# Kernel tuning notes

Measured on AMD Instinct MI355X. Metric: run time of the kernel, lower is better.

## Reference

```python
import jax, jax.numpy as jnp
import numpy as np

NUM_RANGES = 700
K = 250
IN_DIM = 7      # 1 power + 3 elevation embed + 3 azimuth embed
HID = 32        # Q/K hidden dim
NUM_LAYERS = 2
SCALE = 1.0 / (HID ** 0.5)


def setup_inputs() -> dict:
    key = jax.random.key(0)
    ks = jax.random.split(key, 12)
    N = NUM_RANGES * K
    inp = {
        "power_vals": jax.random.normal(ks[0], (N, 1), dtype=jnp.float32),
        "ele_indices": jax.random.randint(ks[1], (N,), 0, 37),
        "azi_indices": jax.random.randint(ks[2], (N,), 0, 107),
        # learned parameters
        "ele_emb": jax.random.normal(ks[3], (37, 3), dtype=jnp.float32),
        "azi_emb": jax.random.normal(ks[4], (107, 3), dtype=jnp.float32),
        # per-layer Q/K/V linear params, stacked over layers
        "Wq": jax.random.normal(ks[5], (NUM_LAYERS, IN_DIM, HID), dtype=jnp.float32) * 0.2,
        "bq": jax.random.normal(ks[6], (NUM_LAYERS, HID), dtype=jnp.float32) * 0.02,
        "Wk": jax.random.normal(ks[7], (NUM_LAYERS, IN_DIM, HID), dtype=jnp.float32) * 0.2,
        "bk": jax.random.normal(ks[8], (NUM_LAYERS, HID), dtype=jnp.float32) * 0.02,
        "Wv": jax.random.normal(ks[9], (NUM_LAYERS, IN_DIM, 1), dtype=jnp.float32) * 0.2,
        "bv": jax.random.normal(ks[10], (NUM_LAYERS, 1), dtype=jnp.float32) * 0.02,
    }
    return inp


def reference(power_vals, ele_indices, azi_indices, ele_emb, azi_emb, Wq, bq, Wk, bk, Wv, bv):
    # x: [R, K, 1]
    x = power_vals.reshape(NUM_RANGES, K, -1)
    # embedding lookups: [R, K, 3]
    e = ele_emb[ele_indices.reshape(NUM_RANGES, K)].astype(jnp.float32)
    a = azi_emb[azi_indices.reshape(NUM_RANGES, K)].astype(jnp.float32)
    for i in range(NUM_LAYERS):
        h = jnp.concatenate([x, e, a], axis=-1)           # [R, K, 7]
        q = h @ Wq[i] + bq[i]                             # [R, K, 32]
        k = h @ Wk[i] + bk[i]                             # [R, K, 32]
        v = h @ Wv[i] + bv[i]                             # [R, K, 1]
        scores = jnp.einsum("rqd,rkd->rqk", q, k) * SCALE  # [R, K, K]
        probs = jax.nn.softmax(scores, axis=-1)
        x = jnp.einsum("rqk,rkd->rqd", probs, v)          # [R, K, 1]
    return x.reshape(NUM_RANGES * K, 1)
```

## Files before the change

### kernel.cpp

```cpp
#include <hip/hip_runtime.h>
#include <hip/hip_fp16.h>

#define NR 700
#define KK 250
#define HID 32

typedef unsigned int uint32;
typedef _Float16 f16x8 __attribute__((ext_vector_type(8)));
typedef float f32x4 __attribute__((ext_vector_type(4)));
typedef _Float16 hpair __attribute__((ext_vector_type(2)));

#if __has_builtin(__builtin_amdgcn_exp2f)
#define EXP2F(x) __builtin_amdgcn_exp2f(x)
#else
#define EXP2F(x) exp2f(x)
#endif

__device__ __forceinline__ uint32 packh2(float lo, float hi) {
    hpair p; p.x = (_Float16)lo; p.y = (_Float16)hi;
    return __builtin_bit_cast(uint32, p);
}
__device__ __forceinline__ f16x8 u4f16(uint4 u) { return __builtin_bit_cast(f16x8, u); }

__device__ __forceinline__ void compute_weights(
    int wt, int l,
    const float* __restrict__ Wq, const float* __restrict__ bq,
    const float* __restrict__ Wk,
    const float* __restrict__ Wv, const float* __restrict__ bv,
    float (*Msh)[7], float* wsh, float* wvsh, float SC2Q)
{
    const float* wq = Wq + l * 7 * HID;
    const float* wk = Wk + l * 7 * HID;
    if (wt < 49) {
        int c = wt / 7, cp = wt % 7;
        float s = 0.f;
        #pragma unroll 8
        for (int d = 0; d < HID; ++d) s = fmaf(wq[c * HID + d], wk[cp * HID + d], s);
        Msh[c][cp] = s * SC2Q;
    } else if (wt < 56) {
        int cp = wt - 49;
        float s = 0.f;
        #pragma unroll 8
        for (int d = 0; d < HID; ++d) s = fmaf(bq[l * HID + d], wk[cp * HID + d], s);
        wsh[cp] = s * SC2Q;
    } else if (wt < 63) {
        wvsh[wt - 56] = Wv[l * 7 + (wt - 56)];
    } else if (wt == 63) {
        wvsh[7] = bv[l];
    }
}

__global__ __launch_bounds__(256, 4) void mlra_kernel(
    const float* __restrict__ power,
    const int*   __restrict__ ele_idx,
    const int*   __restrict__ azi_idx,
    const float* __restrict__ ele_emb,
    const float* __restrict__ azi_emb,
    const float* __restrict__ Wq,
    const float* __restrict__ bq,
    const float* __restrict__ Wk,
    const float* __restrict__ bk,
    const float* __restrict__ Wv,
    const float* __restrict__ bv,
    float* __restrict__ out)
{
    __shared__ uint4 hh[256];
    __shared__ uint4 tt[256];
    __shared__ uint4 vpk[8][4];
    __shared__ float Msh[2][7][7];
    __shared__ float wsh[2][7];
    __shared__ float wvsh[2][8];

    const int r    = blockIdx.x;
    const int tid  = threadIdx.x;
    const int lane = tid & 63;
    const int wid  = tid >> 6;
    const int col  = lane & 15;
    const int grp  = lane >> 4;

    const float SC2Q = 0.17677669529663687f * 1.4426950408889634f * 0.25f;

    {
        float hv[7];
        if (tid < KK) {
            int g = r * KK + tid;
            hv[0] = power[g];
            int ei = ele_idx[g];
            int ai = azi_idx[g];
            hv[1] = ele_emb[ei * 3 + 0];
            hv[2] = ele_emb[ei * 3 + 1];
            hv[3] = ele_emb[ei * 3 + 2];
            hv[4] = azi_emb[ai * 3 + 0];
            hv[5] = azi_emb[ai * 3 + 1];
            hv[6] = azi_emb[ai * 3 + 2];
        } else {
            #pragma unroll
            for (int c = 0; c < 7; ++c) hv[c] = 0.f;
        }
        uint4 u;
        u.x = packh2(hv[0], hv[1]);
        u.y = packh2(hv[2], hv[3]);
        u.z = packh2(hv[4], hv[5]);
        u.w = packh2(hv[6], 0.f);
        hh[tid] = u;
    }
    if (tid < 128) {
        compute_weights(tid & 63, tid >> 6, Wq, bq, Wk, Wv, bv,
                        Msh[tid >> 6], wsh[tid >> 6], wvsh[tid >> 6], SC2Q);
    }
    __syncthreads();

    const f32x4 cz = {0.f, 0.f, 0.f, 0.f};
    float x0 = 0.f, x1 = 0.f, x2 = 0.f, x3 = 0.f;

    for (int l = 0; l < 2; ++l) {
        {
            uint4 u = hh[tid];
            hpair pa = __builtin_bit_cast(hpair, u.x);
            hpair pb = __builtin_bit_cast(hpair, u.y);
            hpair pc = __builtin_bit_cast(hpair, u.z);
            hpair pd = __builtin_bit_cast(hpair, u.w);
            float hv[7] = {(float)pa.x, (float)pa.y, (float)pb.x, (float)pb.y,
                           (float)pc.x, (float)pc.y, (float)pd.x};
            float tv[7];
            #pragma unroll
            for (int cp = 0; cp < 7; ++cp) {
                float s = wsh[l][cp];
                #pragma unroll
                for (int c = 0; c < 7; ++c) s = fmaf(hv[c], Msh[l][c][cp], s);
                tv[cp] = s;
            }
            float v = wvsh[l][7];
            #pragma unroll
            for (int c = 0; c < 7; ++c) v = fmaf(hv[c], wvsh[l][c], v);
            uint4 t4;
            t4.x = packh2(tv[0], tv[1]);
            t4.y = packh2(tv[2], tv[3]);
            t4.z = packh2(tv[4], tv[5]);
            t4.w = packh2(tv[6], 0.f);
            tt[tid] = t4;
            int jtp = tid >> 5, halfsel = (tid >> 4) & 1, grow = (tid >> 2) & 3, rg = tid & 3;
            reinterpret_cast<_Float16*>(vpk)[(jtp * 4 + grow) * 8 + halfsel * 4 + rg] =
                (_Float16)((tid < KK) ? v : 0.f);
        }
        __syncthreads();

        f16x8 bt0 = u4f16(tt[(wid * 4 + 0) * 16 + col]);
        f16x8 bt1 = u4f16(tt[(wid * 4 + 1) * 16 + col]);
        f16x8 bt2 = u4f16(tt[(wid * 4 + 2) * 16 + col]);
        f16x8 bt3 = u4f16(tt[(wid * 4 + 3) * 16 + col]);

        float ss0 = 0.f, oo0 = 0.f, ss1 = 0.f, oo1 = 0.f;
        float ss2 = 0.f, oo2 = 0.f, ss3 = 0.f, oo3 = 0.f;
        #pragma unroll 1
        for (int jtp = 0; jtp < 8; ++jtp) {
            f16x8 ahe = u4f16(hh[jtp * 32 + col]);
            f16x8 aho = u4f16(hh[jtp * 32 + 16 + col]);
            uint4 vq  = vpk[jtp][grp];
            hpair v01e = __builtin_bit_cast(hpair, vq.x);
            hpair v23e = __builtin_bit_cast(hpair, vq.y);
            hpair v01o = __builtin_bit_cast(hpair, vq.z);
            hpair v23o = __builtin_bit_cast(hpair, vq.w);
            float ve0 = (float)v01e.x, ve1 = (float)v01e.y;
            float ve2 = (float)v23e.x, ve3 = (float)v23e.y;
            float vo0 = (float)v01o.x, vo1 = (float)v01o.y;
            float vo2 = (float)v23o.x, vo3 = (float)v23o.y;

            f32x4 ce0 = __builtin_amdgcn_mfma_f32_16x16x32_f16(ahe, bt0, cz, 0, 0, 0);
            f32x4 ce1 = __builtin_amdgcn_mfma_f32_16x16x32_f16(ahe, bt1, cz, 0, 0, 0);
            f32x4 ce2 = __builtin_amdgcn_mfma_f32_16x16x32_f16(ahe, bt2, cz, 0, 0, 0);
            f32x4 ce3 = __builtin_amdgcn_mfma_f32_16x16x32_f16(ahe, bt3, cz, 0, 0, 0);
            f32x4 co0 = __builtin_amdgcn_mfma_f32_16x16x32_f16(aho, bt0, cz, 0, 0, 0);
            f32x4 co1 = __builtin_amdgcn_mfma_f32_16x16x32_f16(aho, bt1, cz, 0, 0, 0);
            f32x4 co2 = __builtin_amdgcn_mfma_f32_16x16x32_f16(aho, bt2, cz, 0, 0, 0);
            f32x4 co3 = __builtin_amdgcn_mfma_f32_16x16x32_f16(aho, bt3, cz, 0, 0, 0);

            #define ACC(ct, vv0, vv1, vv2, vv3, SS, OO)                         \
            {                                                                    \
                float p0 = EXP2F(ct[0]); float p1 = EXP2F(ct[1]);                \
                float p2 = EXP2F(ct[2]); float p3 = EXP2F(ct[3]);                \
                SS += (p0 + p1) + (p2 + p3);                                     \
                OO = fmaf(p0, vv0, OO); OO = fmaf(p1, vv1, OO);                  \
                OO = fmaf(p2, vv2, OO); OO = fmaf(p3, vv3, OO);                  \
            }
            ACC(ce0, ve0, ve1, ve2, ve3, ss0, oo0)
            ACC(ce1, ve0, ve1, ve2, ve3, ss1, oo1)
            ACC(ce2, ve0, ve1, ve2, ve3, ss2, oo2)
            ACC(ce3, ve0, ve1, ve2, ve3, ss3, oo3)
            ACC(co0, vo0, vo1, vo2, vo3, ss0, oo0)
            ACC(co1, vo0, vo1, vo2, vo3, ss1, oo1)
            ACC(co2, vo0, vo1, vo2, vo3, ss2, oo2)
            ACC(co3, vo0, vo1, vo2, vo3, ss3, oo3)
            #undef ACC
        }
        {
            int ex = 4 * grp - 6;
            ex = ex < 0 ? 0 : (ex > 4 ? 4 : ex);
            float exf = (float)ex;
            ss0 -= exf; ss1 -= exf; ss2 -= exf; ss3 -= exf;
        }

        ss0 += __shfl_xor(ss0, 16); ss0 += __shfl_xor(ss0, 32);
        oo0 += __shfl_xor(oo0, 16); oo0 += __shfl_xor(oo0, 32);
        ss1 += __shfl_xor(ss1, 16); ss1 += __shfl_xor(ss1, 32);
        oo1 += __shfl_xor(oo1, 16); oo1 += __shfl_xor(oo1, 32);
        ss2 += __shfl_xor(ss2, 16); ss2 += __shfl_xor(ss2, 32);
        oo2 += __shfl_xor(oo2, 16); oo2 += __shfl_xor(oo2, 32);
        ss3 += __shfl_xor(ss3, 16); ss3 += __shfl_xor(ss3, 32);
        oo3 += __shfl_xor(oo3, 16); oo3 += __shfl_xor(oo3, 32);
        x0 = oo0 / ss0; x1 = oo1 / ss1; x2 = oo2 / ss2; x3 = oo3 / ss3;

        if (l == 0) {
            __syncthreads();
            if (grp == 0) {
                int i0 = (wid * 4 + 0) * 16 + col;
                int i1 = (wid * 4 + 1) * 16 + col;
                int i2 = (wid * 4 + 2) * 16 + col;
                int i3 = (wid * 4 + 3) * 16 + col;
                _Float16* hhf = reinterpret_cast<_Float16*>(hh);
                hhf[i0 * 8] = (_Float16)x0;
                hhf[i1 * 8] = (_Float16)x1;
                hhf[i2 * 8] = (_Float16)x2;
                if (i3 < KK) hhf[i3 * 8] = (_Float16)x3;
            }
            __syncthreads();
        }
    }

    if (grp == 0) {
        int i0 = (wid * 4 + 0) * 16 + col;
        int i1 = (wid * 4 + 1) * 16 + col;
        int i2 = (wid * 4 + 2) * 16 + col;
        int i3 = (wid * 4 + 3) * 16 + col;
        out[r * KK + i0] = x0;
        out[r * KK + i1] = x1;
        out[r * KK + i2] = x2;
        if (i3 < KK) out[r * KK + i3] = x3;
    }
}

extern "C" void kernel_launch(void* const* d_in, const int* in_sizes, int n_in,
                              void* d_out, int out_size, void* d_ws, size_t ws_size,
                              hipStream_t stream) {
    const float* power   = (const float*)d_in[0];
    const int*   ele     = (const int*)d_in[1];
    const int*   azi     = (const int*)d_in[2];
    const float* ele_emb = (const float*)d_in[3];
    const float* azi_emb = (const float*)d_in[4];
    const float* Wq      = (const float*)d_in[5];
    const float* bq      = (const float*)d_in[6];
    const float* Wk      = (const float*)d_in[7];
    const float* bk      = (const float*)d_in[8];
    const float* Wv      = (const float*)d_in[9];
    const float* bv      = (const float*)d_in[10];
    float* outp = (float*)d_out;
    (void)bk;

    hipLaunchKernelGGL(mlra_kernel, dim3(NR), dim3(256), 0, stream,
                       power, ele, azi, ele_emb, azi_emb, Wq, bq, Wk, bk, Wv, bv, outp);
}
```

Measured before the change: 23.37 us.

## Compute softmax P·V and row sums with an extra MFMA instead of scalar FMAs

Exponentiated scores are packed to fp16 and multiplied by a B operand holding V in column 0 and ones in column 1, so one MFMA yields both the weighted sum and the softmax denominator. This replaces per-lane scalar FMA accumulation and cross-lane xor-shuffle reductions with matrix-core work and a single shuffle per output. It adds fp16 rounding of probabilities (round-toward-zero) and leaves a dead macro in the code.

```diff
diff --git a/kernel.cpp b/kernel.cpp
--- a/kernel.cpp
+++ b/kernel.cpp
@@ -21,6 +21,9 @@
     return __builtin_bit_cast(uint32, p);
 }
 __device__ __forceinline__ f16x8 u4f16(uint4 u) { return __builtin_bit_cast(f16x8, u); }
+__device__ __forceinline__ uint32 pkrtz(float a, float b) {
+    return __builtin_bit_cast(uint32, __builtin_amdgcn_cvt_pkrtz(a, b));
+}
 
 __device__ __forceinline__ void compute_weights(
     int wt, int l,
@@ -66,7 +69,7 @@
 {
     __shared__ uint4 hh[256];
     __shared__ uint4 tt[256];
-    __shared__ uint4 vpk[8][4];
+    __shared__ _Float16 vB[8][32];
     __shared__ float Msh[2][7][7];
     __shared__ float wsh[2][7];
     __shared__ float wvsh[2][8];
@@ -76,7 +79,7 @@
     const int lane = tid & 63;
     const int wid  = tid >> 6;
     const int col  = lane & 15;
-    const int grp  = lane >> 4;
+    const int kg   = lane >> 4;
 
     const float SC2Q = 0.17677669529663687f * 1.4426950408889634f * 0.25f;
 
@@ -111,7 +114,7 @@
     __syncthreads();
 
     const f32x4 cz = {0.f, 0.f, 0.f, 0.f};
-    float x0 = 0.f, x1 = 0.f, x2 = 0.f, x3 = 0.f;
+    float xs[4];
 
     for (int l = 0; l < 2; ++l) {
         {
@@ -139,9 +142,10 @@
             t4.z = packh2(tv[4], tv[5]);
             t4.w = packh2(tv[6], 0.f);
             tt[tid] = t4;
-            int jtp = tid >> 5, halfsel = (tid >> 4) & 1, grow = (tid >> 2) & 3, rg = tid & 3;
-            reinterpret_cast<_Float16*>(vpk)[(jtp * 4 + grow) * 8 + halfsel * 4 + rg] =
-                (_Float16)((tid < KK) ? v : 0.f);
+            int jtp = tid >> 5, j32 = tid & 31;
+            int kgw = (j32 & 15) >> 2;
+            int e   = (j32 & 3) + ((j32 >> 4) << 2);
+            vB[jtp][kgw * 8 + e] = (_Float16)((tid < KK) ? v : 0.f);
         }
         __syncthreads();
 
@@ -150,21 +154,20 @@
         f16x8 bt2 = u4f16(tt[(wid * 4 + 2) * 16 + col]);
         f16x8 bt3 = u4f16(tt[(wid * 4 + 3) * 16 + col]);
 
-        float ss0 = 0.f, oo0 = 0.f, ss1 = 0.f, oo1 = 0.f;
-        float ss2 = 0.f, oo2 = 0.f, ss3 = 0.f, oo3 = 0.f;
+        f32x4 cv0 = cz, cv1 = cz, cv2 = cz, cv3 = cz;
+        const uint32 onesm = 0x3C003C00u;
+
         #pragma unroll 1
         for (int jtp = 0; jtp < 8; ++jtp) {
             f16x8 ahe = u4f16(hh[jtp * 32 + col]);
             f16x8 aho = u4f16(hh[jtp * 32 + 16 + col]);
-            uint4 vq  = vpk[jtp][grp];
-            hpair v01e = __builtin_bit_cast(hpair, vq.x);
-            hpair v23e = __builtin_bit_cast(hpair, vq.y);
-            hpair v01o = __builtin_bit_cast(hpair, vq.z);
-            hpair v23o = __builtin_bit_cast(hpair, vq.w);
-            float ve0 = (float)v01e.x, ve1 = (float)v01e.y;
-            float ve2 = (float)v23e.x, ve3 = (float)v23e.y;
-            float vo0 = (float)v01o.x, vo1 = (float)v01o.y;
-            float vo2 = (float)v23o.x, vo3 = (float)v23o.y;
+            uint4 vq = *reinterpret_cast<const uint4*>(&vB[jtp][kg * 8]);
+            uint4 bb;
+            bb.x = (col == 0) ? vq.x : ((col == 1) ? onesm : 0u);
+            bb.y = (col == 0) ? vq.y : ((col == 1) ? onesm : 0u);
+            bb.z = (col == 0) ? vq.z : ((col == 1) ? onesm : 0u);
+            bb.w = (col == 0) ? vq.w : ((col == 1) ? onesm : 0u);
+            f16x8 bf = u4f16(bb);
 
             f32x4 ce0 = __builtin_amdgcn_mfma_f32_16x16x32_f16(ahe, bt0, cz, 0, 0, 0);
             f32x4 ce1 = __builtin_amdgcn_mfma_f32_16x16x32_f16(ahe, bt1, cz, 0, 0, 0);
@@ -175,67 +178,74 @@
             f32x4 co2 = __builtin_amdgcn_mfma_f32_16x16x32_f16(aho, bt2, cz, 0, 0, 0);
             f32x4 co3 = __builtin_amdgcn_mfma_f32_16x16x32_f16(aho, bt3, cz, 0, 0, 0);
 
-            #define ACC(ct, vv0, vv1, vv2, vv3, SS, OO)                         \
+            #define PV(CE, CO, CV)                                               \
             {                                                                    \
-                float p0 = EXP2F(ct[0]); float p1 = EXP2F(ct[1]);                \
-                float p2 = EXP2F(ct[2]); float p3 = EXP2F(ct[3]);                \
-                SS += (p0 + p1) + (p2 + p3);                                     \
-                OO = fmaf(p0, vv0, OO); OO = fmaf(p1, vv1, OO);                  \
-                OO = fmaf(p2, vv2, OO); OO = fmaf(p3, vv3, OO);                  \
-            }
-            ACC(ce0, ve0, ve1, ve2, ve3, ss0, oo0)
-            ACC(ce1, ve0, ve1, ve2, ve3, ss1, oo1)
-            ACC(ce2, ve0, ve1, ve2, ve3, ss2, oo2)
-            ACC(ce3, ve0, ve1, ve2, ve3, ss3, oo3)
-            ACC(co0, vo0, vo1, vo2, vo3, ss0, oo0)
-            ACC(co1, vo0, vo1, vo2, vo3, ss1, oo1)
-            ACC(co2, vo0, vo1, vo2, vo3, ss2, oo2)
-            ACC(co3, vo0, vo1, vo2, vo3, ss3, oo3)
-            #undef ACC
-        }
-        {
-            int ex = 4 * grp - 6;
-            ex = ex < 0 ? 0 : (ex > 4 ? 4 : ex);
-            float exf = (float)ex;
-            ss0 -= exf; ss1 -= exf; ss2 -= exf; ss3 -= exf;
-        }
-
-        ss0 += __shfl_xor(ss0, 16); ss0 += __shfl_xor(ss0, 32);
-        oo0 += __shfl_xor(oo0, 16); oo0 += __shfl_xor(oo0, 32);
-        ss1 += __shfl_xor(ss1, 16); ss1 += __shfl_xor(ss1, 32);
-        oo1 += __shfl_xor(oo1, 16); oo1 += __shfl_xor(oo1, 32);
-        ss2 += __shfl_xor(ss2, 16); ss2 += __shfl_xor(ss2, 32);
-        oo2 += __shfl_xor(oo2, 16); oo2 += __shfl_xor(oo2, 32);
-        ss3 += __shfl_xor(ss3, 16); ss3 += __shfl_xor(ss3, 32);
-        oo3 += __shfl_xor(oo3, 16); oo3 += __shfl_xor(oo3, 32);
-        x0 = oo0 / ss0; x1 = oo1 / ss1; x2 = oo2 / ss2; x3 = oo3 / ss3;
+                float pe0 = EXP2F(CE[0]); float pe1 = EXP2F(CE[1]);              \
+                float pe2 = EXP2F(CE[2]); float pe3 = EXP2F(CE[3]);              \
+                float po0 = EXP2F(CO[0]); float po1 = EXP2F(CO[1]);              \
+                float po2 = EXP2F(CO[2]); float po3 = EXP2F(CO[3]);              \
+                uint4 ua;                                                        \
+                ua.x = pkrtz(pe0, pe1); ua.y = pkrtz(pe2, pe3);                  \
+                ua.z = pkrtz(po0, po1); ua.w = pkrtz(po2, po3);                  \
+                CV = __builtin_amdgcn_mfma_f32_16x16x32_f16(u4f16(ua), bf, CV, 0, 0, 0); \
+            }
+            PV(ce0, co0, cv0)
+            PV(ce1, co1, cv1)
+            PV(ce2, co2, cv2)
+            PV(ce3, co3, cv3)
+            #undef PV
+        }
+
+        #define FIN(CV, T)                                                       \
+        {                                                                        \
+            _Pragma("unroll")                                                    \
+            for (int rg = 0; rg < 4; ++rg) {                                     \
+                float oo = CV[rg];                                               \
+                float ssn = __shfl_xor(CV[rg], 1) - 6.0f;                        \
+                if (rg == 0) xs[T] = oo / ssn;                                   \
+                else if (rg == 1) { if (T >= 0) {} xs[T] = (col == 0) ? xs[T] : xs[T]; } \
+            }                                                                    \
+        }
+        #undef FIN
+        f32x4 xt0, xt1, xt2, xt3;
+        #pragma unroll
+        for (int rg = 0; rg < 4; ++rg) {
+            xt0[rg] = cv0[rg] / (__shfl_xor(cv0[rg], 1) - 6.0f);
+            xt1[rg] = cv1[rg] / (__shfl_xor(cv1[rg], 1) - 6.0f);
+            xt2[rg] = cv2[rg] / (__shfl_xor(cv2[rg], 1) - 6.0f);
+            xt3[rg] = cv3[rg] / (__shfl_xor(cv3[rg], 1) - 6.0f);
+        }
 
         if (l == 0) {
             __syncthreads();
-            if (grp == 0) {
-                int i0 = (wid * 4 + 0) * 16 + col;
-                int i1 = (wid * 4 + 1) * 16 + col;
-                int i2 = (wid * 4 + 2) * 16 + col;
-                int i3 = (wid * 4 + 3) * 16 + col;
+            if (col == 0) {
                 _Float16* hhf = reinterpret_cast<_Float16*>(hh);
-                hhf[i0 * 8] = (_Float16)x0;
-                hhf[i1 * 8] = (_Float16)x1;
-                hhf[i2 * 8] = (_Float16)x2;
-                if (i3 < KK) hhf[i3 * 8] = (_Float16)x3;
+                #pragma unroll
+                for (int rg = 0; rg < 4; ++rg) {
+                    int i0 = (wid * 4 + 0) * 16 + kg * 4 + rg;
+                    int i1 = (wid * 4 + 1) * 16 + kg * 4 + rg;
+                    int i2 = (wid * 4 + 2) * 16 + kg * 4 + rg;
+                    int i3 = (wid * 4 + 3) * 16 + kg * 4 + rg;
+                    hhf[i0 * 8] = (_Float16)xt0[rg];
+                    hhf[i1 * 8] = (_Float16)xt1[rg];
+                    hhf[i2 * 8] = (_Float16)xt2[rg];
+                    if (i3 < KK) hhf[i3 * 8] = (_Float16)xt3[rg];
+                }
             }
             __syncthreads();
-        }
-    }
-
-    if (grp == 0) {
-        int i0 = (wid * 4 + 0) * 16 + col;
-        int i1 = (wid * 4 + 1) * 16 + col;
-        int i2 = (wid * 4 + 2) * 16 + col;
-        int i3 = (wid * 4 + 3) * 16 + col;
-        out[r * KK + i0] = x0;
-        out[r * KK + i1] = x1;
-        out[r * KK + i2] = x2;
-        if (i3 < KK) out[r * KK + i3] = x3;
+        } else if (col == 0) {
+            #pragma unroll
+            for (int rg = 0; rg < 4; ++rg) {
+                int i0 = (wid * 4 + 0) * 16 + kg * 4 + rg;
+                int i1 = (wid * 4 + 1) * 16 + kg * 4 + rg;
+                int i2 = (wid * 4 + 2) * 16 + kg * 4 + rg;
+                int i3 = (wid * 4 + 3) * 16 + kg * 4 + rg;
+                out[r * KK + i0] = xt0[rg];
+                out[r * KK + i1] = xt1[rg];
+                out[r * KK + i2] = xt2[rg];
+                if (i3 < KK) out[r * KK + i3] = xt3[rg];
+            }
+        }
     }
 }
 
```

Result: no change. 23.80 us (+1.8%).

## Split layers into two launches and halve query rows per block

Applied to the files above, without the earlier changes.

The fused two-layer kernel becomes a templated per-layer kernel launched twice. Layer 0's outputs go to an fp16 workspace, and layer 1 re-gathers the embeddings and reads that workspace. Each range is now split across two blocks, each handling half the query tiles, which doubles the grid to 1400 blocks for better CU occupancy. In exchange, the K projection and the embedding gathers are redundantly recomputed per half-block and per layer, and a second kernel launch adds overhead.

```diff
diff --git a/kernel.cpp b/kernel.cpp
--- a/kernel.cpp
+++ b/kernel.cpp
@@ -45,12 +45,13 @@
         wsh[cp] = s * SC2Q;
     } else if (wt < 63) {
         wvsh[wt - 56] = Wv[l * 7 + (wt - 56)];
-    } else if (wt == 63) {
+    } else {
         wvsh[7] = bv[l];
     }
 }
 
-__global__ __launch_bounds__(256, 4) void mlra_kernel(
+template <int LAYER>
+__global__ __launch_bounds__(256, 4) void mlra_layer(
     const float* __restrict__ power,
     const int*   __restrict__ ele_idx,
     const int*   __restrict__ azi_idx,
@@ -59,44 +60,47 @@
     const float* __restrict__ Wq,
     const float* __restrict__ bq,
     const float* __restrict__ Wk,
-    const float* __restrict__ bk,
     const float* __restrict__ Wv,
     const float* __restrict__ bv,
+    _Float16* __restrict__ wsx,
     float* __restrict__ out)
 {
     __shared__ uint4 hh[256];
     __shared__ uint4 tt[256];
     __shared__ uint4 vpk[8][4];
-    __shared__ float Msh[2][7][7];
-    __shared__ float wsh[2][7];
-    __shared__ float wvsh[2][8];
-
-    const int r    = blockIdx.x;
+    __shared__ float Msh[7][7];
+    __shared__ float wsh[7];
+    __shared__ float wvsh[8];
+
+    const int rb   = blockIdx.x;
+    const int r    = rb >> 1;
+    const int half = rb & 1;
     const int tid  = threadIdx.x;
     const int lane = tid & 63;
     const int wid  = tid >> 6;
     const int col  = lane & 15;
-    const int grp  = lane >> 4;
+    const int kg   = lane >> 4;
+    const int tb   = half * 8 + wid * 2;
 
     const float SC2Q = 0.17677669529663687f * 1.4426950408889634f * 0.25f;
 
+    float hv[7];
+    if (tid < KK) {
+        int g = r * KK + tid;
+        hv[0] = (LAYER == 0) ? power[g] : (float)wsx[r * 256 + tid];
+        int ei = ele_idx[g];
+        int ai = azi_idx[g];
+        hv[1] = ele_emb[ei * 3 + 0];
+        hv[2] = ele_emb[ei * 3 + 1];
+        hv[3] = ele_emb[ei * 3 + 2];
+        hv[4] = azi_emb[ai * 3 + 0];
+        hv[5] = azi_emb[ai * 3 + 1];
+        hv[6] = azi_emb[ai * 3 + 2];
+    } else {
+        #pragma unroll
+        for (int c = 0; c < 7; ++c) hv[c] = 0.f;
+    }
     {
-        float hv[7];
-        if (tid < KK) {
-            int g = r * KK + tid;
-            hv[0] = power[g];
-            int ei = ele_idx[g];
-            int ai = azi_idx[g];
-            hv[1] = ele_emb[ei * 3 + 0];
-            hv[2] = ele_emb[ei * 3 + 1];
-            hv[3] = ele_emb[ei * 3 + 2];
-            hv[4] = azi_emb[ai * 3 + 0];
-            hv[5] = azi_emb[ai * 3 + 1];
-            hv[6] = azi_emb[ai * 3 + 2];
-        } else {
-            #pragma unroll
-            for (int c = 0; c < 7; ++c) hv[c] = 0.f;
-        }
         uint4 u;
         u.x = packh2(hv[0], hv[1]);
         u.y = packh2(hv[2], hv[3]);
@@ -104,138 +108,98 @@
         u.w = packh2(hv[6], 0.f);
         hh[tid] = u;
     }
-    if (tid < 128) {
-        compute_weights(tid & 63, tid >> 6, Wq, bq, Wk, Wv, bv,
-                        Msh[tid >> 6], wsh[tid >> 6], wvsh[tid >> 6], SC2Q);
+    if (tid < 64) {
+        compute_weights(tid, LAYER, Wq, bq, Wk, Wv, bv, Msh, wsh, wvsh, SC2Q);
     }
     __syncthreads();
 
+    {
+        float tv[7];
+        #pragma unroll
+        for (int cp = 0; cp < 7; ++cp) {
+            float s = wsh[cp];
+            #pragma unroll
+            for (int c = 0; c < 7; ++c) s = fmaf(hv[c], Msh[c][cp], s);
+            tv[cp] = s;
+        }
+        float v = wvsh[7];
+        #pragma unroll
+        for (int c = 0; c < 7; ++c) v = fmaf(hv[c], wvsh[c], v);
+        uint4 t4;
+        t4.x = packh2(tv[0], tv[1]);
+        t4.y = packh2(tv[2], tv[3]);
+        t4.z = packh2(tv[4], tv[5]);
+        t4.w = packh2(tv[6], 0.f);
+        tt[tid] = t4;
+        int jtp = tid >> 5, halfsel = (tid >> 4) & 1, grow = (tid >> 2) & 3, rg = tid & 3;
+        reinterpret_cast<_Float16*>(vpk)[(jtp * 4 + grow) * 8 + halfsel * 4 + rg] =
+            (_Float16)((tid < KK) ? v : 0.f);
+    }
+    __syncthreads();
+
     const f32x4 cz = {0.f, 0.f, 0.f, 0.f};
-    float x0 = 0.f, x1 = 0.f, x2 = 0.f, x3 = 0.f;
-
-    for (int l = 0; l < 2; ++l) {
-        {
-            uint4 u = hh[tid];
-            hpair pa = __builtin_bit_cast(hpair, u.x);
-            hpair pb = __builtin_bit_cast(hpair, u.y);
-            hpair pc = __builtin_bit_cast(hpair, u.z);
-            hpair pd = __builtin_bit_cast(hpair, u.w);
-            float hv[7] = {(float)pa.x, (float)pa.y, (float)pb.x, (float)pb.y,
-                           (float)pc.x, (float)pc.y, (float)pd.x};
-            float tv[7];
-            #pragma unroll
-            for (int cp = 0; cp < 7; ++cp) {
-                float s = wsh[l][cp];
-                #pragma unroll
-                for (int c = 0; c < 7; ++c) s = fmaf(hv[c], Msh[l][c][cp], s);
-                tv[cp] = s;
-            }
-            float v = wvsh[l][7];
-            #pragma unroll
-            for (int c = 0; c < 7; ++c) v = fmaf(hv[c], wvsh[l][c], v);
-            uint4 t4;
-            t4.x = packh2(tv[0], tv[1]);
-            t4.y = packh2(tv[2], tv[3]);
-            t4.z = packh2(tv[4], tv[5]);
-            t4.w = packh2(tv[6], 0.f);
-            tt[tid] = t4;
-            int jtp = tid >> 5, halfsel = (tid >> 4) & 1, grow = (tid >> 2) & 3, rg = tid & 3;
-            reinterpret_cast<_Float16*>(vpk)[(jtp * 4 + grow) * 8 + halfsel * 4 + rg] =
-                (_Float16)((tid < KK) ? v : 0.f);
+
+    f16x8 bt0 = u4f16(tt[(tb + 0) * 16 + col]);
+    f16x8 bt1 = u4f16(tt[(tb + 1) * 16 + col]);
+
+    float ss0 = 0.f, oo0 = 0.f, ss1 = 0.f, oo1 = 0.f;
+    #pragma unroll 1
+    for (int jtp = 0; jtp < 8; ++jtp) {
+        f16x8 ahe = u4f16(hh[jtp * 32 + col]);
+        f16x8 aho = u4f16(hh[jtp * 32 + 16 + col]);
+        uint4 vq  = vpk[jtp][kg];
+        hpair v01e = __builtin_bit_cast(hpair, vq.x);
+        hpair v23e = __builtin_bit_cast(hpair, vq.y);
+        hpair v01o = __builtin_bit_cast(hpair, vq.z);
+        hpair v23o = __builtin_bit_cast(hpair, vq.w);
+        float ve0 = (float)v01e.x, ve1 = (float)v01e.y;
+        float ve2 = (float)v23e.x, ve3 = (float)v23e.y;
+        float vo0 = (float)v01o.x, vo1 = (float)v01o.y;
+        float vo2 = (float)v23o.x, vo3 = (float)v23o.y;
+
+        f32x4 ce0 = __builtin_amdgcn_mfma_f32_16x16x32_f16(ahe, bt0, cz, 0, 0, 0);
+        f32x4 ce1 = __builtin_amdgcn_mfma_f32_16x16x32_f16(ahe, bt1, cz, 0, 0, 0);
+        f32x4 co0 = __builtin_amdgcn_mfma_f32_16x16x32_f16(aho, bt0, cz, 0, 0, 0);
+        f32x4 co1 = __builtin_amdgcn_mfma_f32_16x16x32_f16(aho, bt1, cz, 0, 0, 0);
+
+        #define ACC(ct, vv0, vv1, vv2, vv3, SS, OO)                         \
+        {                                                                    \
+            float p0 = EXP2F(ct[0]); float p1 = EXP2F(ct[1]);                \
+            float p2 = EXP2F(ct[2]); float p3 = EXP2F(ct[3]);                \
+            SS += (p0 + p1) + (p2 + p3);                                     \
+            OO = fmaf(p0, vv0, OO); OO = fmaf(p1, vv1, OO);                  \
+            OO = fmaf(p2, vv2, OO); OO = fmaf(p3, vv3, OO);                  \
         }
-        __syncthreads();
-
-        f16x8 bt0 = u4f16(tt[(wid * 4 + 0) * 16 + col]);
-        f16x8 bt1 = u4f16(tt[(wid * 4 + 1) * 16 + col]);
-        f16x8 bt2 = u4f16(tt[(wid * 4 + 2) * 16 + col]);
-        f16x8 bt3 = u4f16(tt[(wid * 4 + 3) * 16 + col]);
-
-        float ss0 = 0.f, oo0 = 0.f, ss1 = 0.f, oo1 = 0.f;
-        float ss2 = 0.f, oo2 = 0.f, ss3 = 0.f, oo3 = 0.f;
-        #pragma unroll 1
-        for (int jtp = 0; jtp < 8; ++jtp) {
-            f16x8 ahe = u4f16(hh[jtp * 32 + col]);
-            f16x8 aho = u4f16(hh[jtp * 32 + 16 + col]);
-            uint4 vq  = vpk[jtp][grp];
-            hpair v01e = __builtin_bit_cast(hpair, vq.x);
-            hpair v23e = __builtin_bit_cast(hpair, vq.y);
-            hpair v01o = __builtin_bit_cast(hpair, vq.z);
-            hpair v23o = __builtin_bit_cast(hpair, vq.w);
-            float ve0 = (float)v01e.x, ve1 = (float)v01e.y;
-            float ve2 = (float)v23e.x, ve3 = (float)v23e.y;
-            float vo0 = (float)v01o.x, vo1 = (float)v01o.y;
-            float vo2 = (float)v23o.x, vo3 = (float)v23o.y;
-
-            f32x4 ce0 = __builtin_amdgcn_mfma_f32_16x16x32_f16(ahe, bt0, cz, 0, 0, 0);
-            f32x4 ce1 = __builtin_amdgcn_mfma_f32_16x16x32_f16(ahe, bt1, cz, 0, 0, 0);
-            f32x4 ce2 = __builtin_amdgcn_mfma_f32_16x16x32_f16(ahe, bt2, cz, 0, 0, 0);
-            f32x4 ce3 = __builtin_amdgcn_mfma_f32_16x16x32_f16(ahe, bt3, cz, 0, 0, 0);
-            f32x4 co0 = __builtin_amdgcn_mfma_f32_16x16x32_f16(aho, bt0, cz, 0, 0, 0);
-            f32x4 co1 = __builtin_amdgcn_mfma_f32_16x16x32_f16(aho, bt1, cz, 0, 0, 0);
-            f32x4 co2 = __builtin_amdgcn_mfma_f32_16x16x32_f16(aho, bt2, cz, 0, 0, 0);
-            f32x4 co3 = __builtin_amdgcn_mfma_f32_16x16x32_f16(aho, bt3, cz, 0, 0, 0);
-
-            #define ACC(ct, vv0, vv1, vv2, vv3, SS, OO)                         \
-            {                                                                    \
-                float p0 = EXP2F(ct[0]); float p1 = EXP2F(ct[1]);                \
-                float p2 = EXP2F(ct[2]); float p3 = EXP2F(ct[3]);                \
-                SS += (p0 + p1) + (p2 + p3);                                     \
-                OO = fmaf(p0, vv0, OO); OO = fmaf(p1, vv1, OO);                  \
-                OO = fmaf(p2, vv2, OO); OO = fmaf(p3, vv3, OO);                  \
-            }
-            ACC(ce0, ve0, ve1, ve2, ve3, ss0, oo0)
-            ACC(ce1, ve0, ve1, ve2, ve3, ss1, oo1)
-            ACC(ce2, ve0, ve1, ve2, ve3, ss2, oo2)
-            ACC(ce3, ve0, ve1, ve2, ve3, ss3, oo3)
-            ACC(co0, vo0, vo1, vo2, vo3, ss0, oo0)
-            ACC(co1, vo0, vo1, vo2, vo3, ss1, oo1)
-            ACC(co2, vo0, vo1, vo2, vo3, ss2, oo2)
-            ACC(co3, vo0, vo1, vo2, vo3, ss3, oo3)
-            #undef ACC
+        ACC(ce0, ve0, ve1, ve2, ve3, ss0, oo0)
+        ACC(ce1, ve0, ve1, ve2, ve3, ss1, oo1)
+        ACC(co0, vo0, vo1, vo2, vo3, ss0, oo0)
+        ACC(co1, vo0, vo1, vo2, vo3, ss1, oo1)
+        #undef ACC
+    }
+    {
+        int ex = 4 * kg - 6;
+        ex = ex < 0 ? 0 : (ex > 4 ? 4 : ex);
+        float exf = (float)ex;
+        ss0 -= exf; ss1 -= exf;
+    }
+
+    ss0 += __shfl_xor(ss0, 16); ss0 += __shfl_xor(ss0, 32);
+    oo0 += __shfl_xor(oo0, 16); oo0 += __shfl_xor(oo0, 32);
+    ss1 += __shfl_xor(ss1, 16); ss1 += __shfl_xor(ss1, 32);
+    oo1 += __shfl_xor(oo1, 16); oo1 += __shfl_xor(oo1, 32);
+    float x0 = oo0 / ss0;
+    float x1 = oo1 / ss1;
+
+    if (kg == 0) {
+        int i0 = (tb + 0) * 16 + col;
+        int i1 = (tb + 1) * 16 + col;
+        if (LAYER == 0) {
+            wsx[r * 256 + i0] = (_Float16)x0;
+            wsx[r * 256 + i1] = (_Float16)((i1 < KK) ? x1 : 0.f);
+        } else {
+            out[r * KK + i0] = x0;
+            if (i1 < KK) out[r * KK + i1] = x1;
         }
-        {
-            int ex = 4 * grp - 6;
-            ex = ex < 0 ? 0 : (ex > 4 ? 4 : ex);
-            float exf = (float)ex;
-            ss0 -= exf; ss1 -= exf; ss2 -= exf; ss3 -= exf;
-        }
-
-        ss0 += __shfl_xor(ss0, 16); ss0 += __shfl_xor(ss0, 32);
-        oo0 += __shfl_xor(oo0, 16); oo0 += __shfl_xor(oo0, 32);
-        ss1 += __shfl_xor(ss1, 16); ss1 += __shfl_xor(ss1, 32);
-        oo1 += __shfl_xor(oo1, 16); oo1 += __shfl_xor(oo1, 32);
-        ss2 += __shfl_xor(ss2, 16); ss2 += __shfl_xor(ss2, 32);
-        oo2 += __shfl_xor(oo2, 16); oo2 += __shfl_xor(oo2, 32);
-        ss3 += __shfl_xor(ss3, 16); ss3 += __shfl_xor(ss3, 32);
-        oo3 += __shfl_xor(oo3, 16); oo3 += __shfl_xor(oo3, 32);
-        x0 = oo0 / ss0; x1 = oo1 / ss1; x2 = oo2 / ss2; x3 = oo3 / ss3;
-
-        if (l == 0) {
-            __syncthreads();
-            if (grp == 0) {
-                int i0 = (wid * 4 + 0) * 16 + col;
-                int i1 = (wid * 4 + 1) * 16 + col;
-                int i2 = (wid * 4 + 2) * 16 + col;
-                int i3 = (wid * 4 + 3) * 16 + col;
-                _Float16* hhf = reinterpret_cast<_Float16*>(hh);
-                hhf[i0 * 8] = (_Float16)x0;
-                hhf[i1 * 8] = (_Float16)x1;
-                hhf[i2 * 8] = (_Float16)x2;
-                if (i3 < KK) hhf[i3 * 8] = (_Float16)x3;
-            }
-            __syncthreads();
-        }
-    }
-
-    if (grp == 0) {
-        int i0 = (wid * 4 + 0) * 16 + col;
-        int i1 = (wid * 4 + 1) * 16 + col;
-        int i2 = (wid * 4 + 2) * 16 + col;
-        int i3 = (wid * 4 + 3) * 16 + col;
-        out[r * KK + i0] = x0;
-        out[r * KK + i1] = x1;
-        out[r * KK + i2] = x2;
-        if (i3 < KK) out[r * KK + i3] = x3;
     }
 }
 
@@ -254,8 +218,11 @@
     const float* Wv      = (const float*)d_in[9];
     const float* bv      = (const float*)d_in[10];
     float* outp = (float*)d_out;
-    (void)bk;
-
-    hipLaunchKernelGGL(mlra_kernel, dim3(NR), dim3(256), 0, stream,
-                       power, ele, azi, ele_emb, azi_emb, Wq, bq, Wk, bk, Wv, bv, outp);
-}
+    _Float16* wsx = (_Float16*)d_ws;
+    (void)bk; (void)ws_size;
+
+    hipLaunchKernelGGL((mlra_layer<0>), dim3(2 * NR), dim3(256), 0, stream,
+                       power, ele, azi, ele_emb, azi_emb, Wq, bq, Wk, Wv, bv, wsx, outp);
+    hipLaunchKernelGGL((mlra_layer<1>), dim3(2 * NR), dim3(256), 0, stream,
+                       power, ele, azi, ele_emb, azi_emb, Wq, bq, Wk, Wv, bv, wsx, outp);
+}
```

Result: slower. 27.91 us (+19.4%).
